# Kernel optimization log

Measured on AMD Instinct MI355X. Metric: run time of the kernel, lower is better.

The kernel has to match this reference:

```python
import jax, jax.numpy as jnp
import numpy as np

N_NODES = 100000

def setup_inputs() -> dict:
    key = jax.random.key(0)
    k1, k2, k3, k4 = jax.random.split(key, 4)
    E = 1600000
    x = jax.random.normal(k1, (N_NODES, 128), dtype=jnp.float32)
    src = jax.random.randint(k2, (E,), 0, N_NODES, dtype=jnp.int32)
    dst = jax.random.randint(k3, (E,), 0, N_NODES, dtype=jnp.int32)
    W = jax.random.normal(k4, (128, 128), dtype=jnp.float32) * (1.0 / np.sqrt(128.0))
    b = jnp.zeros((128,), dtype=jnp.float32)
    return {"x": x, "src": src, "dst": dst, "W": W, "b": b}

def reference(x, src, dst, W, b):
    # DGL GraphConv, norm='both', allow_zero_in_degree=True
    N = x.shape[0]
    ones = jnp.ones_like(src, dtype=x.dtype)
    out_deg = jax.ops.segment_sum(ones, src, num_segments=N)
    in_deg = jax.ops.segment_sum(ones, dst, num_segments=N)
    out_norm = jnp.power(jnp.clip(out_deg, 1.0), -0.5)  # [N]
    in_norm = jnp.power(jnp.clip(in_deg, 1.0), -0.5)    # [N]
    h = x * out_norm[:, None]                            # [N, d]
    msg = h[src]                                         # [E, d] gather
    agg = jax.ops.segment_sum(msg, dst, num_segments=N)  # [N, d] scatter-sum
    agg = agg * in_norm[:, None]
    return agg @ W + b
```

## Files before the change

kernel.cpp:

```cpp
#include <hip/hip_runtime.h>

#define NFEAT 128
#define BSHIFT 9
#define BNODES 512
#define NBMAX 256
#define BCAP 9216
#define CHUNK 2048

typedef __attribute__((ext_vector_type(8))) short bf16x8;
typedef __attribute__((ext_vector_type(4))) float f32x4;
typedef unsigned short u16;

__device__ inline u16 f2bf(float f) {
    unsigned u = __float_as_uint(f);
    u += 0x7FFF + ((u >> 16) & 1);
    return (u16)(u >> 16);
}
__device__ inline float bf2f(u16 h) {
    return __uint_as_float((unsigned)h << 16);
}

__global__ __launch_bounds__(256)
void partition_kernel(const int* __restrict__ src, const int* __restrict__ dst, int E,
                      int* __restrict__ cursor, int* __restrict__ packed,
                      int* __restrict__ out_deg, int NB) {
    __shared__ int cnt[NBMAX];
    for (int i = threadIdx.x; i < NB; i += 256) cnt[i] = 0;
    __syncthreads();
    int base = blockIdx.x * CHUNK;
    int end = min(base + CHUNK, E);
    for (int j = base + threadIdx.x; j < end; j += 256) {
        atomicAdd(&out_deg[src[j]], 1);
        atomicAdd(&cnt[dst[j] >> BSHIFT], 1);
    }
    __syncthreads();
    for (int i = threadIdx.x; i < NB; i += 256) {
        int c = cnt[i];
        cnt[i] = c ? (i * BCAP + atomicAdd(&cursor[i], c)) : 0;
    }
    __syncthreads();
    for (int j = base + threadIdx.x; j < end; j += 256) {
        int d = dst[j];
        int b = d >> BSHIFT;
        int pos = atomicAdd(&cnt[b], 1);
        packed[pos] = ((d & (BNODES - 1)) << 17) | src[j];
    }
}

__global__ void csr_scan_kernel(const int* __restrict__ cursor,
                                int* __restrict__ csr_base, int NB) {
    __shared__ int sa[256], sb[256];
    int tid = threadIdx.x;
    int v = (tid < NB) ? cursor[tid] : 0;
    sa[tid] = v;
    __syncthreads();
    int* s = sa; int* t = sb;
    for (int d = 1; d < 256; d <<= 1) {
        t[tid] = s[tid] + (tid >= d ? s[tid - d] : 0);
        __syncthreads();
        int* tmp = s; s = t; t = tmp;
    }
    if (tid < NB) csr_base[tid] = s[tid] - v;
    if (tid == 255) csr_base[NB] = s[255];
}

__global__ __launch_bounds__(512)
void fill_cast_kernel(const int* __restrict__ packed, const int* __restrict__ cursor,
                      const int* __restrict__ csr_base,
                      int* __restrict__ row_start, float* __restrict__ inorm,
                      int* __restrict__ csr_src,
                      const float* __restrict__ x, const int* __restrict__ out_deg,
                      u16* __restrict__ xh, const float* __restrict__ W,
                      u16* __restrict__ Wt, int N, int E, int NB, int nbc) {
    int bid = blockIdx.x;
    int tid = threadIdx.x;

    if (bid < NB) {
        __shared__ int cnt[BNODES];
        __shared__ int sa[BNODES], sb[BNODES];
        int bkt = bid;
        int node0 = bkt << BSHIFT;
        int nn = min(BNODES, N - node0);
        int beg = bkt * BCAP;
        int ccnt = cursor[bkt];
        int csr0 = csr_base[bkt];

        cnt[tid] = 0;
        __syncthreads();
        for (int i = tid; i < ccnt; i += 512)
            atomicAdd(&cnt[packed[beg + i] >> 17], 1);
        __syncthreads();

        int v = cnt[tid];
        sa[tid] = v;
        __syncthreads();
        int* s = sa; int* t = sb;
        for (int d = 1; d < 512; d <<= 1) {
            t[tid] = s[tid] + (tid >= d ? s[tid - d] : 0);
            __syncthreads();
            int* tmp = s; s = t; t = tmp;
        }
        int excl = s[tid] - v;

        if (tid < nn) {
            row_start[node0 + tid] = csr0 + excl;
            inorm[node0 + tid] = rsqrtf((float)max(v, 1));
        }
        if (bkt == 0 && tid == 0) row_start[N] = E;
        __syncthreads();

        cnt[tid] = csr0 + excl;
        __syncthreads();
        for (int i = tid; i < ccnt; i += 512) {
            int p = packed[beg + i];
            int slot = atomicAdd(&cnt[p >> 17], 1);
            csr_src[slot] = p & 0x1FFFF;
        }
    } else if (bid < NB + nbc) {
        int node0 = (bid - NB) << 7;
        for (int i = tid; i < 128 * 32; i += 512) {
            int r = i >> 5, f4 = i & 31;
            int n = node0 + r;
            if (n >= N) break;
            float sc = rsqrtf((float)max(out_deg[n], 1));
            float4 vv = *reinterpret_cast<const float4*>(&x[(size_t)n * NFEAT + f4 * 4]);
            ushort4 o;
            o.x = f2bf(vv.x * sc); o.y = f2bf(vv.y * sc);
            o.z = f2bf(vv.z * sc); o.w = f2bf(vv.w * sc);
            *reinterpret_cast<ushort4*>(&xh[(size_t)n * NFEAT + f4 * 4]) = o;
        }
    } else {
        for (int i = tid; i < NFEAT * NFEAT; i += 512) {
            int col = i >> 7, k = i & 127;
            Wt[i] = f2bf(W[k * NFEAT + col]);
        }
    }
}

__global__ __launch_bounds__(256)
void agg_bf16_kernel(const u16* __restrict__ xh, const int* __restrict__ csr_src,
                     const int* __restrict__ row_start, const float* __restrict__ inorm,
                     u16* __restrict__ aggh, int N) {
    int node = blockIdx.x * 8 + (threadIdx.x >> 5);
    if (node >= N) return;
    int lf = threadIdx.x & 31;
    int beg = row_start[node];
    int end = row_start[node + 1];
    const ushort4* xr = reinterpret_cast<const ushort4*>(xh);

    float4 acc = make_float4(0.f, 0.f, 0.f, 0.f);
    for (int i = beg; i < end; i += 8) {
        int s[8];
        float m[8];
        #pragma unroll
        for (int u = 0; u < 8; ++u) {
            int j = i + u;
            bool ok = (j < end);
            s[u] = ok ? csr_src[j] : 0;
            m[u] = ok ? 1.f : 0.f;
        }
        ushort4 v[8];
        #pragma unroll
        for (int u = 0; u < 8; ++u)
            v[u] = xr[(size_t)s[u] * 32 + lf];
        #pragma unroll
        for (int u = 0; u < 8; ++u) {
            acc.x = fmaf(m[u], bf2f(v[u].x), acc.x);
            acc.y = fmaf(m[u], bf2f(v[u].y), acc.y);
            acc.z = fmaf(m[u], bf2f(v[u].z), acc.z);
            acc.w = fmaf(m[u], bf2f(v[u].w), acc.w);
        }
    }
    float in_n = inorm[node];
    ushort4 o;
    o.x = f2bf(acc.x * in_n);
    o.y = f2bf(acc.y * in_n);
    o.z = f2bf(acc.z * in_n);
    o.w = f2bf(acc.w * in_n);
    *reinterpret_cast<ushort4*>(aggh + (size_t)node * 256 + lf * 4) = o;
}

__global__ __launch_bounds__(256)
void mm_mfma_kernel(const u16* __restrict__ aggh, float* outp,
                    const u16* __restrict__ Wt, const float* __restrict__ b, int N) {
    __shared__ u16 Al[NFEAT * NFEAT];
    __shared__ u16 Bl[NFEAT * NFEAT];
    int tid = threadIdx.x;
    int r0 = blockIdx.x * 128;

    for (int c = tid; c < 2048; c += 256) {
        int col = c >> 4, sub = c & 15;
        int slot = sub ^ (col & 7);
        *reinterpret_cast<uint4*>(reinterpret_cast<char*>(Bl) + col * 256 + slot * 16) =
            *reinterpret_cast<const uint4*>(reinterpret_cast<const char*>(Wt) + c * 16);
    }
    for (int c = tid; c < 2048; c += 256) {
        int row = c >> 4, sub = c & 15;
        int grow = min(r0 + row, N - 1);
        int slot = sub ^ (row & 7);
        *reinterpret_cast<uint4*>(reinterpret_cast<char*>(Al) + row * 256 + slot * 16) =
            *reinterpret_cast<const uint4*>(reinterpret_cast<const char*>(aggh) +
                                            (size_t)grow * 512 + sub * 16);
    }
    __syncthreads();

    int lane = tid & 63;
    int wave = tid >> 6;
    int wr = wave >> 1, wc = wave & 1;
    int lrow = lane & 15, hi = lane >> 4;

    f32x4 zero = {0.f, 0.f, 0.f, 0.f};
    f32x4 acc[4][4];
    #pragma unroll
    for (int rt = 0; rt < 4; ++rt)
        #pragma unroll
        for (int ct = 0; ct < 4; ++ct) acc[rt][ct] = zero;

    #pragma unroll
    for (int ks = 0; ks < 4; ++ks) {
        int chunk = ks * 4 + hi;
        bf16x8 af[4], bfr[4];
        #pragma unroll
        for (int rt = 0; rt < 4; ++rt) {
            int row = wr * 64 + rt * 16 + lrow;
            af[rt] = *reinterpret_cast<bf16x8*>(reinterpret_cast<char*>(Al) + row * 256 +
                                                ((chunk ^ (row & 7)) * 16));
        }
        #pragma unroll
        for (int ct = 0; ct < 4; ++ct) {
            int col = wc * 64 + ct * 16 + lrow;
            bfr[ct] = *reinterpret_cast<bf16x8*>(reinterpret_cast<char*>(Bl) + col * 256 +
                                                 ((chunk ^ (col & 7)) * 16));
        }
        #pragma unroll
        for (int rt = 0; rt < 4; ++rt)
            #pragma unroll
            for (int ct = 0; ct < 4; ++ct)
                acc[rt][ct] = __builtin_amdgcn_mfma_f32_16x16x32_bf16(af[rt], bfr[ct],
                                                                     acc[rt][ct], 0, 0, 0);
    }

    #pragma unroll
    for (int ct = 0; ct < 4; ++ct) {
        int col = wc * 64 + ct * 16 + lrow;
        float bias = b[col];
        #pragma unroll
        for (int rt = 0; rt < 4; ++rt) {
            int rbase = r0 + wr * 64 + rt * 16 + hi * 4;
            #pragma unroll
            for (int q = 0; q < 4; ++q) {
                int row = rbase + q;
                if (row < N) outp[(size_t)row * NFEAT + col] = acc[rt][ct][q] + bias;
            }
        }
    }
}

extern "C" void kernel_launch(void* const* d_in, const int* in_sizes, int n_in,
                              void* d_out, int out_size, void* d_ws, size_t ws_size,
                              hipStream_t stream) {
    const float* x   = (const float*)d_in[0];
    const int*   src = (const int*)d_in[1];
    const int*   dst = (const int*)d_in[2];
    const float* W   = (const float*)d_in[3];
    const float* b   = (const float*)d_in[4];

    const int N = in_sizes[0] / NFEAT;
    const int E = in_sizes[1];
    float* out = (float*)d_out;

    const int NB = (N + BNODES - 1) >> BSHIFT;

    int*   out_deg   = (int*)d_ws;
    int*   cursor    = out_deg + N;
    int*   csr_base  = cursor + NBMAX;
    int*   row_start = csr_base + (NBMAX + 1);
    float* inorm     = (float*)(row_start + (N + 1));
    int*   csr_src   = (int*)(inorm + N);
    u16*   Wt        = (u16*)(csr_src + E);
    u16*   xh        = Wt + NFEAT * NFEAT;

    int* packed = (int*)d_out;

    hipMemsetAsync(d_ws, 0, (size_t)(N + NBMAX) * sizeof(int), stream);

    int nchunk = (E + CHUNK - 1) / CHUNK;
    partition_kernel<<<nchunk, 256, 0, stream>>>(src, dst, E, cursor, packed, out_deg, NB);
    csr_scan_kernel<<<1, 256, 0, stream>>>(cursor, csr_base, NB);

    int nbc = (N + 127) >> 7;
    fill_cast_kernel<<<NB + nbc + 1, 512, 0, stream>>>(packed, cursor, csr_base,
                                                       row_start, inorm, csr_src,
                                                       x, out_deg, xh, W, Wt, N, E, NB, nbc);

    u16* aggh = (u16*)d_out;
    agg_bf16_kernel<<<(N + 7) / 8, 256, 0, stream>>>(xh, csr_src, row_start, inorm, aggh, N);

    mm_mfma_kernel<<<(N + 127) / 128, 256, 0, stream>>>(aggh, out, Wt, b, N);
}
```

Measured before the change: 232.3 us.

## Locally sort edges in shared memory before bucket scatter; split out-degree kernel

The partition kernel now counting-sorts each chunk of edges by destination bucket in shared memory, then writes them out in bucket order so global stores to each bucket are contiguous rather than scattered. Chunk size and block size are doubled. The out-degree atomics move into a separate grid-stride kernel. This adds an extra kernel launch, an in-block scan and more shared memory per block, in exchange for better-coalesced writes to the packed array.

```diff
diff --git a/kernel.cpp b/kernel.cpp
--- a/kernel.cpp
+++ b/kernel.cpp
@@ -5,7 +5,7 @@
 #define BNODES 512
 #define NBMAX 256
 #define BCAP 9216
-#define CHUNK 2048
+#define CHUNK 4096
 
 typedef __attribute__((ext_vector_type(8))) short bf16x8;
 typedef __attribute__((ext_vector_type(4))) float f32x4;
@@ -21,29 +21,63 @@
 }
 
 __global__ __launch_bounds__(256)
+void deg_kernel(const int* __restrict__ src, int E, int* __restrict__ out_deg) {
+    int stride = gridDim.x * 256;
+    for (int i = blockIdx.x * 256 + threadIdx.x; i < E; i += stride)
+        atomicAdd(&out_deg[src[i]], 1);
+}
+
+__global__ __launch_bounds__(512)
 void partition_kernel(const int* __restrict__ src, const int* __restrict__ dst, int E,
-                      int* __restrict__ cursor, int* __restrict__ packed,
-                      int* __restrict__ out_deg, int NB) {
+                      int* __restrict__ cursor, int* __restrict__ packed, int NB) {
     __shared__ int cnt[NBMAX];
-    for (int i = threadIdx.x; i < NB; i += 256) cnt[i] = 0;
-    __syncthreads();
+    __shared__ int loff[NBMAX];
+    __shared__ int gbase[NBMAX];
+    __shared__ int sa[NBMAX], sb[NBMAX];
+    __shared__ int sortv[CHUNK];
+    __shared__ u16 sortb[CHUNK];
+
+    int tid = threadIdx.x;
+    if (tid < NBMAX) cnt[tid] = 0;
+    __syncthreads();
+
     int base = blockIdx.x * CHUNK;
-    int end = min(base + CHUNK, E);
-    for (int j = base + threadIdx.x; j < end; j += 256) {
-        atomicAdd(&out_deg[src[j]], 1);
+    int endj = min(base + CHUNK, E);
+    int ccnt = endj - base;
+
+    for (int j = base + tid; j < endj; j += 512)
         atomicAdd(&cnt[dst[j] >> BSHIFT], 1);
-    }
-    __syncthreads();
-    for (int i = threadIdx.x; i < NB; i += 256) {
-        int c = cnt[i];
-        cnt[i] = c ? (i * BCAP + atomicAdd(&cursor[i], c)) : 0;
-    }
-    __syncthreads();
-    for (int j = base + threadIdx.x; j < end; j += 256) {
-        int d = dst[j];
-        int b = d >> BSHIFT;
-        int pos = atomicAdd(&cnt[b], 1);
-        packed[pos] = ((d & (BNODES - 1)) << 17) | src[j];
+    __syncthreads();
+
+    int v = (tid < NBMAX) ? cnt[tid] : 0;
+    if (tid < NBMAX) sa[tid] = v;
+    __syncthreads();
+    int* s = sa; int* t = sb;
+    for (int d = 1; d < NBMAX; d <<= 1) {
+        if (tid < NBMAX) t[tid] = s[tid] + (tid >= d ? s[tid - d] : 0);
+        __syncthreads();
+        int* tmp = s; s = t; t = tmp;
+    }
+    if (tid < NBMAX) {
+        int excl = s[tid] - v;
+        loff[tid] = excl;
+        cnt[tid] = excl;
+        gbase[tid] = v ? (tid * BCAP + atomicAdd(&cursor[tid], v)) : 0;
+    }
+    __syncthreads();
+
+    for (int j = base + tid; j < endj; j += 512) {
+        int d_ = dst[j];
+        int bkt = d_ >> BSHIFT;
+        int pos = atomicAdd(&cnt[bkt], 1);
+        sortv[pos] = ((d_ & (BNODES - 1)) << 17) | src[j];
+        sortb[pos] = (u16)bkt;
+    }
+    __syncthreads();
+
+    for (int p = tid; p < ccnt; p += 512) {
+        int bkt = sortb[p];
+        packed[gbase[bkt] + (p - loff[bkt])] = sortv[p];
     }
 }
 
@@ -284,8 +318,10 @@
 
     hipMemsetAsync(d_ws, 0, (size_t)(N + NBMAX) * sizeof(int), stream);
 
+    deg_kernel<<<2048, 256, 0, stream>>>(src, E, out_deg);
+
     int nchunk = (E + CHUNK - 1) / CHUNK;
-    partition_kernel<<<nchunk, 256, 0, stream>>>(src, dst, E, cursor, packed, out_deg, NB);
+    partition_kernel<<<nchunk, 512, 0, stream>>>(src, dst, E, cursor, packed, NB);
     csr_scan_kernel<<<1, 256, 0, stream>>>(cursor, csr_base, NB);
 
     int nbc = (N + 127) >> 7;
```

After: 227.5 us. 2.1% less time.
